# Performance work log

Hardware: AMD Instinct MI355X
Metric: run time of the kernel (lower is better)

Reference implementation:

```python
import jax, jax.numpy as jnp
import numpy as np

T, C, H = 2048, 1024, 16
D = C // H  # head dim = 64


def setup_inputs() -> dict:
    key = jax.random.key(0)
    k1, k2, k3 = jax.random.split(key, 3)
    x = jax.random.normal(k1, (T, C), dtype=jnp.float32)
    W_qkv = jax.random.normal(k2, (C, 3 * C), dtype=jnp.float32) * (1.0 / np.sqrt(C))
    b_qkv = jnp.zeros((3 * C,), dtype=jnp.float32)
    W_proj = jax.random.normal(k3, (C, C), dtype=jnp.float32) * (1.0 / np.sqrt(C))
    b_proj = jnp.zeros((C,), dtype=jnp.float32)
    return {"x": x, "W_qkv": W_qkv, "b_qkv": b_qkv, "W_proj": W_proj, "b_proj": b_proj}


def reference(x, W_qkv, b_qkv, W_proj, b_proj):
    t, c = x.shape
    qkv = x @ W_qkv + b_qkv                      # [T, 3C] fused QKV projection
    q, k, v = jnp.split(qkv, 3, axis=-1)         # each [T, C]
    # split heads: [T, C] -> [H, T, D]
    q = q.reshape(t, H, D).transpose(1, 0, 2)
    k = k.reshape(t, H, D).transpose(1, 0, 2)
    v = v.reshape(t, H, D).transpose(1, 0, 2)
    # naive O(T^2) attention, full score matrix [H, T, T]
    att = jnp.einsum('htd,hsd->hts', q, k) / jnp.sqrt(jnp.float32(D))
    att = jax.nn.softmax(att, axis=-1)
    y = jnp.einsum('hts,hsd->htd', att, v)       # [H, T, D]
    y = y.transpose(1, 0, 2).reshape(t, c)       # merge heads -> [T, C]
    return y @ W_proj + b_proj
```

## Files before the change

kernel.cpp:

```cpp
#include <hip/hip_runtime.h>
#include <hip/hip_bf16.h>
#include <stdint.h>

#define T_DIM 2048
#define C_DIM 1024
#define H_DIM 16
#define D_HEAD 64
#define N_QKV 3072
#define CQ 0.18033688011112042f

typedef __bf16 bf16;
typedef __bf16 bf16x8 __attribute__((ext_vector_type(8)));
typedef __bf16 bf16x4 __attribute__((ext_vector_type(4)));
typedef __bf16 bf16x2 __attribute__((ext_vector_type(2)));
typedef float f32x4 __attribute__((ext_vector_type(4)));
typedef short s16x4 __attribute__((ext_vector_type(4)));

__device__ __forceinline__ void lds_load16(const void* g, void* l) {
    __builtin_amdgcn_global_load_lds(
        (const __attribute__((address_space(1))) void*)g,
        (__attribute__((address_space(3))) void*)l, 16, 0, 0);
}

__device__ __forceinline__ f32x4 mfma16(bf16x4 a, bf16x4 b, f32x4 c) {
#if __has_builtin(__builtin_amdgcn_mfma_f32_16x16x16_bf16)
    return __builtin_amdgcn_mfma_f32_16x16x16_bf16(a, b, c, 0, 0, 0);
#elif __has_builtin(__builtin_amdgcn_mfma_f32_16x16x16bf16_1k)
    union { bf16x4 v; s16x4 s; } ua, ub;
    ua.v = a; ub.v = b;
    return __builtin_amdgcn_mfma_f32_16x16x16bf16_1k(ua.s, ub.s, c, 0, 0, 0);
#else
    asm volatile("v_mfma_f32_16x16x16_bf16 %0, %1, %2, %0"
                 : "+v"(c) : "v"(a), "v"(b));
    return c;
#endif
}

__global__ void prep_kernel(const float* __restrict__ x, bf16* __restrict__ xb,
                            const float* __restrict__ Wq, bf16* __restrict__ WqT,
                            const float* __restrict__ Wp, bf16* __restrict__ WpT) {
    __shared__ float tile[32][33];
    int bid = blockIdx.x;
    int t = threadIdx.x;
    if (bid < 1024) {
        int i = (bid * 256 + t) * 8;
        float4 a = *(const float4*)(x + i);
        float4 b = *(const float4*)(x + i + 4);
        bf16x8 o;
        o[0] = (bf16)a.x; o[1] = (bf16)a.y; o[2] = (bf16)a.z; o[3] = (bf16)a.w;
        o[4] = (bf16)b.x; o[5] = (bf16)b.y; o[6] = (bf16)b.z; o[7] = (bf16)b.w;
        *(bf16x8*)(xb + i) = o;
        return;
    }
    bid -= 1024;
    const float* in; bf16* out; int N, nb, kb;
    if (bid < 3072) { in = Wq; out = WqT; N = N_QKV; nb = (bid % 96) * 32; kb = (bid / 96) * 32; }
    else { bid -= 3072; in = Wp; out = WpT; N = C_DIM; nb = (bid % 32) * 32; kb = (bid / 32) * 32; }
    int r = t >> 3, c4 = (t & 7) * 4;
    float4 v = *(const float4*)(in + (size_t)(kb + r) * N + nb + c4);
    tile[r][c4 + 0] = v.x; tile[r][c4 + 1] = v.y;
    tile[r][c4 + 2] = v.z; tile[r][c4 + 3] = v.w;
    __syncthreads();
    bf16x4 ov;
    ov[0] = (bf16)tile[c4 + 0][r]; ov[1] = (bf16)tile[c4 + 1][r];
    ov[2] = (bf16)tile[c4 + 2][r]; ov[3] = (bf16)tile[c4 + 3][r];
    *(bf16x4*)(out + (size_t)(nb + r) * C_DIM + kb + c4) = ov;
}

__global__ __launch_bounds__(256, 3) void qkv_gemm_kernel(
    const bf16* __restrict__ A, const bf16* __restrict__ Bt,
    const float* __restrict__ bias, bf16* __restrict__ qkv)
{
    __shared__ __align__(16) bf16 As[2][128 * 32];
    __shared__ __align__(16) bf16 Bs[2][64 * 32];
    const int bid = blockIdx.x;
    const int xcd = bid & 7, slot = bid >> 3;
    const int rowBase = (slot / 6) * 128;
    const int colBase = (xcd * 6 + (slot % 6)) * 64;
    const int tid = threadIdx.x, lane = tid & 63, w = tid >> 6;
    const int lo16 = lane & 15, quad = lane >> 4;
    const int wm = (w & 1) * 64, wn = (w >> 1) * 32;

    const bf16* ga = A  + (size_t)(rowBase + w * 16 + (lane >> 2)) * C_DIM + (lane & 3) * 8;
    const bf16* gb = Bt + (size_t)(colBase + w * 16 + (lane >> 2)) * C_DIM + (lane & 3) * 8;

    f32x4 acc[4][2] = {};

    for (int k0 = 0; k0 < C_DIM; k0 += 64) {
        __syncthreads();
        #pragma unroll
        for (int p = 0; p < 2; ++p) {
            lds_load16(ga + k0 + p * 32, &As[p][(w * 16) * 32]);
            lds_load16(ga + (size_t)64 * C_DIM + k0 + p * 32, &As[p][(64 + w * 16) * 32]);
            lds_load16(gb + k0 + p * 32, &Bs[p][(w * 16) * 32]);
        }
        __syncthreads();
        #pragma unroll
        for (int p = 0; p < 2; ++p) {
            bf16x8 af[4], bfr[2];
            #pragma unroll
            for (int mi = 0; mi < 4; ++mi) af[mi]  = *(const bf16x8*)&As[p][(wm + mi * 16 + lo16) * 32 + quad * 8];
            #pragma unroll
            for (int ni = 0; ni < 2; ++ni) bfr[ni] = *(const bf16x8*)&Bs[p][(wn + ni * 16 + lo16) * 32 + quad * 8];
            #pragma unroll
            for (int mi = 0; mi < 4; ++mi)
                #pragma unroll
                for (int ni = 0; ni < 2; ++ni)
                    acc[mi][ni] = __builtin_amdgcn_mfma_f32_16x16x32_bf16(af[mi], bfr[ni], acc[mi][ni], 0, 0, 0);
        }
    }

    const float scale = (colBase < C_DIM) ? CQ : 1.0f;
    #pragma unroll
    for (int ni = 0; ni < 2; ++ni) {
        int col = colBase + wn + ni * 16 + lo16;
        float bv = bias[col];
        #pragma unroll
        for (int mi = 0; mi < 4; ++mi) {
            int row0 = rowBase + wm + mi * 16 + quad * 4;
            #pragma unroll
            for (int r = 0; r < 4; ++r)
                qkv[(size_t)(row0 + r) * N_QKV + col] = (bf16)((acc[mi][ni][r] + bv) * scale);
        }
    }
}

__global__ __launch_bounds__(512, 2) void flash_kernel(
    const bf16* __restrict__ qkv,
    bf16* __restrict__ y)
{
    __shared__ union {
        __align__(16) bf16 Vt[4][64][38];
        float Ored[8][16][66];
    } u;
    __shared__ float lred[8][64];

    const int bid = blockIdx.x;
    const int xcd = bid & 7, slot = bid >> 3;
    const int h = xcd * 2 + (slot & 1);
    const int qb = slot >> 1;
    const int tid  = threadIdx.x;
    const int lane = tid & 63, w = tid >> 6;
    const int lo16 = lane & 15, quad = lane >> 4;

    bf16x8 qf[4][2];
    #pragma unroll
    for (int nq = 0; nq < 4; ++nq)
        #pragma unroll
        for (int dk = 0; dk < 2; ++dk)
            qf[nq][dk] = *(const bf16x8*)(qkv + (size_t)(qb * 64 + nq * 16 + lo16) * N_QKV
                                          + h * D_HEAD + dk * 32 + quad * 8);

    f32x4 o_t[4][4] = {};
    float l_acc[4] = {};

    const bf16* kfb = qkv + (size_t)(w * 16 + lo16) * N_QKV + C_DIM + h * D_HEAD + quad * 8;
    const unsigned short* vb16 = (const unsigned short*)(qkv + 2 * C_DIM + h * D_HEAD);

    bf16x8 kf0 = *(const bf16x8*)(kfb);
    bf16x8 kf1 = *(const bf16x8*)(kfb + 32);
    unsigned short vreg[16];
    #pragma unroll
    for (int i = 0; i < 16; ++i)
        vreg[i] = vb16[(size_t)(w * 16 + i) * N_QKV + lane];

    bf16* vdst = &u.Vt[w >> 1][lane][(w & 1) * 16];

    for (int kt = 0; kt < T_DIM / 128; ++kt) {
        union { bf16x8 v; unsigned short us[8]; } p0, p1;
        #pragma unroll
        for (int i = 0; i < 8; ++i) { p0.us[i] = vreg[i]; p1.us[i] = vreg[8 + i]; }
        *(bf16x8*)vdst       = p0.v;
        *(bf16x8*)(vdst + 8) = p1.v;

        bf16x8 nkf0 = kf0, nkf1 = kf1;
        if (kt + 1 < T_DIM / 128) {
            const bf16* kp = kfb + (size_t)(kt + 1) * 128 * N_QKV;
            nkf0 = *(const bf16x8*)(kp);
            nkf1 = *(const bf16x8*)(kp + 32);
            #pragma unroll
            for (int i = 0; i < 16; ++i)
                vreg[i] = vb16[(size_t)((kt + 1) * 128 + w * 16 + i) * N_QKV + lane];
        }

        f32x4 st[4];
        #pragma unroll
        for (int nq = 0; nq < 4; ++nq) {
            f32x4 z = {};
            z = __builtin_amdgcn_mfma_f32_16x16x32_bf16(kf0, qf[nq][0], z, 0, 0, 0);
            st[nq] = __builtin_amdgcn_mfma_f32_16x16x32_bf16(kf1, qf[nq][1], z, 0, 0, 0);
        }

        bf16x4 pb[4];
        #pragma unroll
        for (int nq = 0; nq < 4; ++nq)
            #pragma unroll
            for (int r = 0; r < 4; ++r) {
                float p = __builtin_amdgcn_exp2f(st[nq][r]);
                l_acc[nq] += p;
                pb[nq][r] = (bf16)p;
            }

        bf16x4 vf[4];
        #pragma unroll
        for (int mi = 0; mi < 4; ++mi)
            vf[mi] = *(const bf16x4*)&u.Vt[w >> 1][mi * 16 + lo16][(w & 1) * 16 + quad * 4];

        #pragma unroll
        for (int mi = 0; mi < 4; ++mi)
            #pragma unroll
            for (int nq = 0; nq < 4; ++nq)
                o_t[mi][nq] = mfma16(vf[mi], pb[nq], o_t[mi][nq]);

        kf0 = nkf0; kf1 = nkf1;
    }

    #pragma unroll
    for (int nq = 0; nq < 4; ++nq) {
        l_acc[nq] += __shfl_xor(l_acc[nq], 16);
        l_acc[nq] += __shfl_xor(l_acc[nq], 32);
        if (quad == 0) lred[w][nq * 16 + lo16] = l_acc[nq];
    }

    const int q8 = tid >> 3, dh = tid & 7;
    float linv = 0.f;
    #pragma unroll
    for (int mi = 0; mi < 4; ++mi) {
        __syncthreads();
        #pragma unroll
        for (int nq = 0; nq < 4; ++nq)
            #pragma unroll
            for (int r = 0; r < 4; ++r)
                u.Ored[w][quad * 4 + r][nq * 16 + lo16] = o_t[mi][nq][r];
        __syncthreads();
        if (mi == 0) {
            float ls = 0.f;
            #pragma unroll
            for (int j = 0; j < 8; ++j) ls += lred[j][q8];
            linv = 1.0f / ls;
        }
        bf16x2 ov;
        #pragma unroll
        for (int dj = 0; dj < 2; ++dj) {
            int d = dh * 2 + dj;
            float s = 0.f;
            #pragma unroll
            for (int j = 0; j < 8; ++j) s += u.Ored[j][d][q8];
            ov[dj] = (bf16)(s * linv);
        }
        *(bf16x2*)&y[(size_t)(qb * 64 + q8) * C_DIM + h * D_HEAD + mi * 16 + dh * 2] = ov;
    }
}

__global__ __launch_bounds__(256, 4) void proj_gemm_kernel(
    const bf16* __restrict__ A, const bf16* __restrict__ Bt,
    const float* __restrict__ bias, float* __restrict__ out)
{
    __shared__ __align__(16) bf16 As[2][64 * 32];
    __shared__ __align__(16) bf16 Bs[2][64 * 32];
    const int bid = blockIdx.x;
    const int xcd = bid & 7, slot = bid >> 3;
    const int colBase = (xcd * 2 + (slot & 1)) * 64;
    const int rowBase = (slot >> 1) * 64;
    const int tid = threadIdx.x, lane = tid & 63, w = tid >> 6;
    const int lo16 = lane & 15, quad = lane >> 4;
    const int wm = (w & 1) * 32, wn = (w >> 1) * 32;

    const bf16* ga = A  + (size_t)(rowBase + w * 16 + (lane >> 2)) * C_DIM + (lane & 3) * 8;
    const bf16* gb = Bt + (size_t)(colBase + w * 16 + (lane >> 2)) * C_DIM + (lane & 3) * 8;

    f32x4 acc[2][2] = {};

    for (int k0 = 0; k0 < C_DIM; k0 += 64) {
        __syncthreads();
        #pragma unroll
        for (int p = 0; p < 2; ++p) {
            lds_load16(ga + k0 + p * 32, &As[p][(w * 16) * 32]);
            lds_load16(gb + k0 + p * 32, &Bs[p][(w * 16) * 32]);
        }
        __syncthreads();
        #pragma unroll
        for (int p = 0; p < 2; ++p) {
            bf16x8 af[2], bfr[2];
            #pragma unroll
            for (int mi = 0; mi < 2; ++mi) af[mi]  = *(const bf16x8*)&As[p][(wm + mi * 16 + lo16) * 32 + quad * 8];
            #pragma unroll
            for (int ni = 0; ni < 2; ++ni) bfr[ni] = *(const bf16x8*)&Bs[p][(wn + ni * 16 + lo16) * 32 + quad * 8];
            #pragma unroll
            for (int mi = 0; mi < 2; ++mi)
                #pragma unroll
                for (int ni = 0; ni < 2; ++ni)
                    acc[mi][ni] = __builtin_amdgcn_mfma_f32_16x16x32_bf16(af[mi], bfr[ni], acc[mi][ni], 0, 0, 0);
        }
    }

    #pragma unroll
    for (int ni = 0; ni < 2; ++ni) {
        int col = colBase + wn + ni * 16 + lo16;
        float bv = bias[col];
        #pragma unroll
        for (int mi = 0; mi < 2; ++mi) {
            int row0 = rowBase + wm + mi * 16 + quad * 4;
            #pragma unroll
            for (int r = 0; r < 4; ++r)
                out[(size_t)(row0 + r) * C_DIM + col] = acc[mi][ni][r] + bv;
        }
    }
}

extern "C" void kernel_launch(void* const* d_in, const int* in_sizes, int n_in,
                              void* d_out, int out_size, void* d_ws, size_t ws_size,
                              hipStream_t stream) {
    const float* x      = (const float*)d_in[0];
    const float* W_qkv  = (const float*)d_in[1];
    const float* b_qkv  = (const float*)d_in[2];
    const float* W_proj = (const float*)d_in[3];
    const float* b_proj = (const float*)d_in[4];
    float* out = (float*)d_out;

    char* ws = (char*)d_ws;
    bf16* xb      = (bf16*)(ws);
    bf16* Wqkv_t  = (bf16*)(ws + (4  << 20));
    bf16* Wproj_t = (bf16*)(ws + (10 << 20));
    bf16* qkv_bf  = (bf16*)(ws + (12 << 20));
    bf16* yb      = (bf16*)(ws + (24 << 20));

    prep_kernel<<<5120, 256, 0, stream>>>(x, xb, W_qkv, Wqkv_t, W_proj, Wproj_t);

    qkv_gemm_kernel<<<768, 256, 0, stream>>>(xb, Wqkv_t, b_qkv, qkv_bf);

    flash_kernel<<<512, 512, 0, stream>>>(qkv_bf, yb);

    proj_gemm_kernel<<<512, 256, 0, stream>>>(yb, Wproj_t, b_proj, out);
}
```

Before: 146.1 us.

## Double-buffer V tile in LDS and prefetch two steps ahead in flash loop

Converts the flash attention inner loop to a two-stage software pipeline. V goes into a double-buffered LDS tile: the next tile's V is written while the current one is read, and V global loads are issued two iterations ahead. The loop is unrolled by two with a macro, and s_setprio raises wave priority around the MFMA blocks. This aims to hide global-load and LDS latency behind matrix math, at the cost of doubled LDS for V and more register pressure.

Measured after the change: 166.2 us. +13.8%, slower.

```diff
diff --git a/kernel.cpp b/kernel.cpp
--- a/kernel.cpp
+++ b/kernel.cpp
@@ -125,12 +125,66 @@
     }
 }
 
+#define NKT (T_DIM / 128)
+
+#define FLASH_STEP(KT, RB, WB)                                                        \
+    {                                                                                 \
+        bf16x8 nkf0 = kf0, nkf1 = kf1;                                                \
+        if ((KT) + 1 < NKT) {                                                         \
+            const bf16* kp = kfb + (size_t)((KT) + 1) * 128 * N_QKV;                  \
+            nkf0 = *(const bf16x8*)(kp);                                              \
+            nkf1 = *(const bf16x8*)(kp + 32);                                         \
+        }                                                                             \
+        f32x4 st[4];                                                                  \
+        __builtin_amdgcn_s_setprio(1);                                                \
+        _Pragma("unroll")                                                             \
+        for (int nq = 0; nq < 4; ++nq) {                                              \
+            f32x4 z = {};                                                             \
+            z = __builtin_amdgcn_mfma_f32_16x16x32_bf16(kf0, qf[nq][0], z, 0, 0, 0);  \
+            st[nq] = __builtin_amdgcn_mfma_f32_16x16x32_bf16(kf1, qf[nq][1], z, 0, 0, 0); \
+        }                                                                             \
+        __builtin_amdgcn_s_setprio(0);                                                \
+        bf16x4 vf[4];                                                                 \
+        _Pragma("unroll")                                                             \
+        for (int mi = 0; mi < 4; ++mi)                                                \
+            vf[mi] = *(const bf16x4*)(vrd##RB + mi * 16 * 38);                        \
+        if ((KT) + 1 < NKT) {                                                         \
+            union { bf16x8 v; unsigned short us[8]; } p0, p1;                         \
+            _Pragma("unroll")                                                         \
+            for (int i = 0; i < 8; ++i) { p0.us[i] = vreg[i]; p1.us[i] = vreg[8 + i]; } \
+            *(bf16x8*)(vwr##WB)     = p0.v;                                           \
+            *(bf16x8*)(vwr##WB + 8) = p1.v;                                           \
+            if ((KT) + 2 < NKT) {                                                     \
+                _Pragma("unroll")                                                     \
+                for (int i = 0; i < 16; ++i)                                          \
+                    vreg[i] = vb16[(size_t)(((KT) + 2) * 128 + w * 16 + i) * N_QKV + lane]; \
+            }                                                                         \
+        }                                                                             \
+        bf16x4 pb[4];                                                                 \
+        _Pragma("unroll")                                                             \
+        for (int nq = 0; nq < 4; ++nq)                                                \
+            _Pragma("unroll")                                                         \
+            for (int r = 0; r < 4; ++r) {                                             \
+                float p = __builtin_amdgcn_exp2f(st[nq][r]);                          \
+                l_acc[nq] += p;                                                       \
+                pb[nq][r] = (bf16)p;                                                  \
+            }                                                                         \
+        __builtin_amdgcn_s_setprio(1);                                                \
+        _Pragma("unroll")                                                             \
+        for (int mi = 0; mi < 4; ++mi)                                                \
+            _Pragma("unroll")                                                         \
+            for (int nq = 0; nq < 4; ++nq)                                            \
+                o_t[mi][nq] = mfma16(vf[mi], pb[nq], o_t[mi][nq]);                    \
+        __builtin_amdgcn_s_setprio(0);                                                \
+        kf0 = nkf0; kf1 = nkf1;                                                       \
+    }
+
 __global__ __launch_bounds__(512, 2) void flash_kernel(
     const bf16* __restrict__ qkv,
     bf16* __restrict__ y)
 {
     __shared__ union {
-        __align__(16) bf16 Vt[4][64][38];
+        __align__(16) bf16 Vt[2][4][64][38];
         float Ored[8][16][66];
     } u;
     __shared__ float lred[8][64];
@@ -157,62 +211,31 @@
     const bf16* kfb = qkv + (size_t)(w * 16 + lo16) * N_QKV + C_DIM + h * D_HEAD + quad * 8;
     const unsigned short* vb16 = (const unsigned short*)(qkv + 2 * C_DIM + h * D_HEAD);
 
+    const bf16* vrd0 = &u.Vt[0][w >> 1][lo16][(w & 1) * 16 + quad * 4];
+    const bf16* vrd1 = &u.Vt[1][w >> 1][lo16][(w & 1) * 16 + quad * 4];
+    bf16* vwr0 = &u.Vt[0][w >> 1][lane][(w & 1) * 16];
+    bf16* vwr1 = &u.Vt[1][w >> 1][lane][(w & 1) * 16];
+
+    unsigned short vreg[16];
+    #pragma unroll
+    for (int i = 0; i < 16; ++i)
+        vreg[i] = vb16[(size_t)(w * 16 + i) * N_QKV + lane];
     bf16x8 kf0 = *(const bf16x8*)(kfb);
     bf16x8 kf1 = *(const bf16x8*)(kfb + 32);
-    unsigned short vreg[16];
-    #pragma unroll
-    for (int i = 0; i < 16; ++i)
-        vreg[i] = vb16[(size_t)(w * 16 + i) * N_QKV + lane];
-
-    bf16* vdst = &u.Vt[w >> 1][lane][(w & 1) * 16];
-
-    for (int kt = 0; kt < T_DIM / 128; ++kt) {
+    {
         union { bf16x8 v; unsigned short us[8]; } p0, p1;
         #pragma unroll
         for (int i = 0; i < 8; ++i) { p0.us[i] = vreg[i]; p1.us[i] = vreg[8 + i]; }
-        *(bf16x8*)vdst       = p0.v;
-        *(bf16x8*)(vdst + 8) = p1.v;
-
-        bf16x8 nkf0 = kf0, nkf1 = kf1;
-        if (kt + 1 < T_DIM / 128) {
-            const bf16* kp = kfb + (size_t)(kt + 1) * 128 * N_QKV;
-            nkf0 = *(const bf16x8*)(kp);
-            nkf1 = *(const bf16x8*)(kp + 32);
-            #pragma unroll
-            for (int i = 0; i < 16; ++i)
-                vreg[i] = vb16[(size_t)((kt + 1) * 128 + w * 16 + i) * N_QKV + lane];
-        }
-
-        f32x4 st[4];
-        #pragma unroll
-        for (int nq = 0; nq < 4; ++nq) {
-            f32x4 z = {};
-            z = __builtin_amdgcn_mfma_f32_16x16x32_bf16(kf0, qf[nq][0], z, 0, 0, 0);
-            st[nq] = __builtin_amdgcn_mfma_f32_16x16x32_bf16(kf1, qf[nq][1], z, 0, 0, 0);
-        }
-
-        bf16x4 pb[4];
-        #pragma unroll
-        for (int nq = 0; nq < 4; ++nq)
-            #pragma unroll
-            for (int r = 0; r < 4; ++r) {
-                float p = __builtin_amdgcn_exp2f(st[nq][r]);
-                l_acc[nq] += p;
-                pb[nq][r] = (bf16)p;
-            }
-
-        bf16x4 vf[4];
-        #pragma unroll
-        for (int mi = 0; mi < 4; ++mi)
-            vf[mi] = *(const bf16x4*)&u.Vt[w >> 1][mi * 16 + lo16][(w & 1) * 16 + quad * 4];
-
-        #pragma unroll
-        for (int mi = 0; mi < 4; ++mi)
-            #pragma unroll
-            for (int nq = 0; nq < 4; ++nq)
-                o_t[mi][nq] = mfma16(vf[mi], pb[nq], o_t[mi][nq]);
-
-        kf0 = nkf0; kf1 = nkf1;
+        *(bf16x8*)(vwr0)     = p0.v;
+        *(bf16x8*)(vwr0 + 8) = p1.v;
+        #pragma unroll
+        for (int i = 0; i < 16; ++i)
+            vreg[i] = vb16[(size_t)(128 + w * 16 + i) * N_QKV + lane];
+    }
+
+    for (int kt = 0; kt < NKT; kt += 2) {
+        FLASH_STEP(kt,     0, 1);
+        FLASH_STEP(kt + 1, 1, 0);
     }
 
     #pragma unroll
@@ -324,7 +347,7 @@
     bf16* Wproj_t = (bf16*)(ws + (10 << 20));
     bf16* qkv_bf  = (bf16*)(ws + (12 << 20));
     bf16* yb      = (bf16*)(ws + (24 << 20));
-
+    
     prep_kernel<<<5120, 256, 0, stream>>>(x, xb, W_qkv, Wqkv_t, W_proj, Wproj_t);
 
     qkv_gemm_kernel<<<768, 256, 0, stream>>>(xb, Wqkv_t, b_qkv, qkv_bf);
```

## Double-buffer LDS tiles in QKV and projection GEMMs, raise MFMA priority in flash

Applied to the files above, without the earlier changes.

Both GEMM kernels now hold two LDS buffers. The global-to-LDS load for the next k-slice is issued before the MFMAs on the current slice, and one vmcnt wait plus one barrier replaces the two syncthreads per iteration. This is meant to hide global load latency behind compute. The cost is twice the shared memory, which can lower occupancy, most likely for the 3-blocks-per-CU QKV kernel. The flash kernel also raises wave priority around its PV MFMA block.

Measured after the change: 148.8 us. About the same (+1.8%).

```diff
diff --git a/kernel.cpp b/kernel.cpp
--- a/kernel.cpp
+++ b/kernel.cpp
@@ -67,12 +67,42 @@
     *(bf16x4*)(out + (size_t)(nb + r) * C_DIM + kb + c4) = ov;
 }
 
+#define QKV_STAGE(BUF, K0) do {                                              \
+    lds_load16(ga + (K0),                  &As[BUF][0][(w * 16) * 32]);      \
+    lds_load16(ga + (K0) + 32,             &As[BUF][1][(w * 16) * 32]);      \
+    lds_load16(ga + (size_t)64 * C_DIM + (K0),      &As[BUF][0][(64 + w * 16) * 32]); \
+    lds_load16(ga + (size_t)64 * C_DIM + (K0) + 32, &As[BUF][1][(64 + w * 16) * 32]); \
+    lds_load16(gb + (K0),                  &Bs[BUF][0][(w * 16) * 32]);      \
+    lds_load16(gb + (K0) + 32,             &Bs[BUF][1][(w * 16) * 32]);      \
+} while (0)
+
+#define QKV_COMPUTE(BUF) do {                                                \
+    _Pragma("unroll")                                                        \
+    for (int p = 0; p < 2; ++p) {                                            \
+        bf16x8 af[4], bfr[2];                                                \
+        _Pragma("unroll")                                                    \
+        for (int mi = 0; mi < 4; ++mi) af[mi]  = *(const bf16x8*)&As[BUF][p][(wm + mi * 16 + lo16) * 32 + quad * 8]; \
+        _Pragma("unroll")                                                    \
+        for (int ni = 0; ni < 2; ++ni) bfr[ni] = *(const bf16x8*)&Bs[BUF][p][(wn + ni * 16 + lo16) * 32 + quad * 8]; \
+        _Pragma("unroll")                                                    \
+        for (int mi = 0; mi < 4; ++mi)                                       \
+            _Pragma("unroll")                                                \
+            for (int ni = 0; ni < 2; ++ni)                                   \
+                acc[mi][ni] = __builtin_amdgcn_mfma_f32_16x16x32_bf16(af[mi], bfr[ni], acc[mi][ni], 0, 0, 0); \
+    }                                                                        \
+} while (0)
+
+#define WAIT_AND_BARRIER() do {                                              \
+    asm volatile("s_waitcnt vmcnt(0)" ::: "memory");                         \
+    __builtin_amdgcn_s_barrier();                                            \
+} while (0)
+
 __global__ __launch_bounds__(256, 3) void qkv_gemm_kernel(
     const bf16* __restrict__ A, const bf16* __restrict__ Bt,
     const float* __restrict__ bias, bf16* __restrict__ qkv)
 {
-    __shared__ __align__(16) bf16 As[2][128 * 32];
-    __shared__ __align__(16) bf16 Bs[2][64 * 32];
+    __shared__ __align__(16) bf16 As[2][2][128 * 32];
+    __shared__ __align__(16) bf16 Bs[2][2][64 * 32];
     const int bid = blockIdx.x;
     const int xcd = bid & 7, slot = bid >> 3;
     const int rowBase = (slot / 6) * 128;
@@ -86,28 +116,16 @@
 
     f32x4 acc[4][2] = {};
 
-    for (int k0 = 0; k0 < C_DIM; k0 += 64) {
-        __syncthreads();
-        #pragma unroll
-        for (int p = 0; p < 2; ++p) {
-            lds_load16(ga + k0 + p * 32, &As[p][(w * 16) * 32]);
-            lds_load16(ga + (size_t)64 * C_DIM + k0 + p * 32, &As[p][(64 + w * 16) * 32]);
-            lds_load16(gb + k0 + p * 32, &Bs[p][(w * 16) * 32]);
-        }
-        __syncthreads();
-        #pragma unroll
-        for (int p = 0; p < 2; ++p) {
-            bf16x8 af[4], bfr[2];
-            #pragma unroll
-            for (int mi = 0; mi < 4; ++mi) af[mi]  = *(const bf16x8*)&As[p][(wm + mi * 16 + lo16) * 32 + quad * 8];
-            #pragma unroll
-            for (int ni = 0; ni < 2; ++ni) bfr[ni] = *(const bf16x8*)&Bs[p][(wn + ni * 16 + lo16) * 32 + quad * 8];
-            #pragma unroll
-            for (int mi = 0; mi < 4; ++mi)
-                #pragma unroll
-                for (int ni = 0; ni < 2; ++ni)
-                    acc[mi][ni] = __builtin_amdgcn_mfma_f32_16x16x32_bf16(af[mi], bfr[ni], acc[mi][ni], 0, 0, 0);
-        }
+    QKV_STAGE(0, 0);
+    WAIT_AND_BARRIER();
+
+    for (int k0 = 0; k0 < C_DIM; k0 += 128) {
+        QKV_STAGE(1, k0 + 64);
+        QKV_COMPUTE(0);
+        WAIT_AND_BARRIER();
+        if (k0 + 128 < C_DIM) QKV_STAGE(0, k0 + 128);
+        QKV_COMPUTE(1);
+        WAIT_AND_BARRIER();
     }
 
     const float scale = (colBase < C_DIM) ? CQ : 1.0f;
@@ -206,11 +224,13 @@
         for (int mi = 0; mi < 4; ++mi)
             vf[mi] = *(const bf16x4*)&u.Vt[w >> 1][mi * 16 + lo16][(w & 1) * 16 + quad * 4];
 
+        __builtin_amdgcn_s_setprio(1);
         #pragma unroll
         for (int mi = 0; mi < 4; ++mi)
             #pragma unroll
             for (int nq = 0; nq < 4; ++nq)
                 o_t[mi][nq] = mfma16(vf[mi], pb[nq], o_t[mi][nq]);
+        __builtin_amdgcn_s_setprio(0);
 
         kf0 = nkf0; kf1 = nkf1;
     }
@@ -252,12 +272,35 @@
     }
 }
 
+#define PROJ_STAGE(BUF, K0) do {                                             \
+    lds_load16(ga + (K0),      &As[BUF][0][(w * 16) * 32]);                  \
+    lds_load16(ga + (K0) + 32, &As[BUF][1][(w * 16) * 32]);                  \
+    lds_load16(gb + (K0),      &Bs[BUF][0][(w * 16) * 32]);                  \
+    lds_load16(gb + (K0) + 32, &Bs[BUF][1][(w * 16) * 32]);                  \
+} while (0)
+
+#define PROJ_COMPUTE(BUF) do {                                               \
+    _Pragma("unroll")                                                        \
+    for (int p = 0; p < 2; ++p) {                                            \
+        bf16x8 af[2], bfr[2];                                                \
+        _Pragma("unroll")                                                    \
+        for (int mi = 0; mi < 2; ++mi) af[mi]  = *(const bf16x8*)&As[BUF][p][(wm + mi * 16 + lo16) * 32 + quad * 8]; \
+        _Pragma("unroll")                                                    \
+        for (int ni = 0; ni < 2; ++ni) bfr[ni] = *(const bf16x8*)&Bs[BUF][p][(wn + ni * 16 + lo16) * 32 + quad * 8]; \
+        _Pragma("unroll")                                                    \
+        for (int mi = 0; mi < 2; ++mi)                                       \
+            _Pragma("unroll")                                                \
+            for (int ni = 0; ni < 2; ++ni)                                   \
+                acc[mi][ni] = __builtin_amdgcn_mfma_f32_16x16x32_bf16(af[mi], bfr[ni], acc[mi][ni], 0, 0, 0); \
+    }                                                                        \
+} while (0)
+
 __global__ __launch_bounds__(256, 4) void proj_gemm_kernel(
     const bf16* __restrict__ A, const bf16* __restrict__ Bt,
     const float* __restrict__ bias, float* __restrict__ out)
 {
-    __shared__ __align__(16) bf16 As[2][64 * 32];
-    __shared__ __align__(16) bf16 Bs[2][64 * 32];
+    __shared__ __align__(16) bf16 As[2][2][64 * 32];
+    __shared__ __align__(16) bf16 Bs[2][2][64 * 32];
     const int bid = blockIdx.x;
     const int xcd = bid & 7, slot = bid >> 3;
     const int colBase = (xcd * 2 + (slot & 1)) * 64;
@@ -271,27 +314,16 @@
 
     f32x4 acc[2][2] = {};
 
-    for (int k0 = 0; k0 < C_DIM; k0 += 64) {
-        __syncthreads();
-        #pragma unroll
-        for (int p = 0; p < 2; ++p) {
-            lds_load16(ga + k0 + p * 32, &As[p][(w * 16) * 32]);
-            lds_load16(gb + k0 + p * 32, &Bs[p][(w * 16) * 32]);
-        }
-        __syncthreads();
-        #pragma unroll
-        for (int p = 0; p < 2; ++p) {
-            bf16x8 af[2], bfr[2];
-            #pragma unroll
-            for (int mi = 0; mi < 2; ++mi) af[mi]  = *(const bf16x8*)&As[p][(wm + mi * 16 + lo16) * 32 + quad * 8];
-            #pragma unroll
-            for (int ni = 0; ni < 2; ++ni) bfr[ni] = *(const bf16x8*)&Bs[p][(wn + ni * 16 + lo16) * 32 + quad * 8];
-            #pragma unroll
-            for (int mi = 0; mi < 2; ++mi)
-                #pragma unroll
-                for (int ni = 0; ni < 2; ++ni)
-                    acc[mi][ni] = __builtin_amdgcn_mfma_f32_16x16x32_bf16(af[mi], bfr[ni], acc[mi][ni], 0, 0, 0);
-        }
+    PROJ_STAGE(0, 0);
+    WAIT_AND_BARRIER();
+
+    for (int k0 = 0; k0 < C_DIM; k0 += 128) {
+        PROJ_STAGE(1, k0 + 64);
+        PROJ_COMPUTE(0);
+        WAIT_AND_BARRIER();
+        if (k0 + 128 < C_DIM) PROJ_STAGE(0, k0 + 128);
+        PROJ_COMPUTE(1);
+        WAIT_AND_BARRIER();
     }
 
     #pragma unroll
```
